# Kernel tuning notes

Measured on AMD Instinct MI355X. Metric: run time of the kernel, lower is better.

Reference implementation:

```python
import jax, jax.numpy as jnp
import numpy as np
import math

HIDDEN = 1024
N_HEADS = 16
N_KV = 4
HEAD_DIM = HIDDEN // N_HEADS  # 64
B, S = 2, 2048
THETA = 100000.0


def _freqs_cos_sin(dim, end, theta):
    # yarn params: original_max_position_embeddings=2048 >= end, so no ramp scaling,
    # attention_factor=1.0 -> plain RoPE frequencies.
    inv = 1.0 / theta ** (np.arange(0, dim, 2)[: dim // 2] / dim)
    t = np.arange(end)
    f = np.outer(t, inv).astype(np.float32)  # (end, dim/2)
    cos = np.concatenate([np.cos(f), np.cos(f)], axis=-1)  # (end, dim)
    sin = np.concatenate([np.sin(f), np.sin(f)], axis=-1)
    return jnp.asarray(cos), jnp.asarray(sin)


def _rotate(x):
    # stack([-x[...,1::2], x[...,::2]], -1).reshape_as(x)
    return jnp.stack([-x[..., 1::2], x[..., ::2]], axis=-1).reshape(x.shape)


def setup_inputs() -> dict:
    key = jax.random.key(0)
    ks = jax.random.split(key, 9)
    s = 0.02
    return {
        "hidden_states": jax.random.normal(ks[0], (B, S, HIDDEN), jnp.float32),
        "attention_mask": jnp.ones((B, S), jnp.int32),
        "Wq": jax.random.normal(ks[1], (HIDDEN, HIDDEN), jnp.float32) * s,
        "bq": jnp.zeros((HIDDEN,), jnp.float32),
        "Wk": jax.random.normal(ks[2], (HIDDEN, N_KV * HEAD_DIM), jnp.float32) * s,
        "bk": jnp.zeros((N_KV * HEAD_DIM,), jnp.float32),
        "Wv": jax.random.normal(ks[3], (HIDDEN, N_KV * HEAD_DIM), jnp.float32) * s,
        "bv": jnp.zeros((N_KV * HEAD_DIM,), jnp.float32),
        "Wo": jax.random.normal(ks[4], (HIDDEN, HIDDEN), jnp.float32) * s,
        "bo": jnp.zeros((HIDDEN,), jnp.float32),
    }


def reference(hidden_states, attention_mask, Wq, bq, Wk, bk, Wv, bv, Wo, bo):
    b, s, _ = hidden_states.shape
    q = (hidden_states @ Wq + bq).reshape(b, s, N_HEADS, HEAD_DIM)
    k = (hidden_states @ Wk + bk).reshape(b, s, N_KV, HEAD_DIM)
    v = (hidden_states @ Wv + bv).reshape(b, s, N_KV, HEAD_DIM)

    cos, sin = _freqs_cos_sin(HEAD_DIM, s, THETA)
    cos = cos[:, None, :]  # (s,1,d) broadcasts over (b,s,h,d)
    sin = sin[:, None, :]
    q = q * cos + _rotate(q) * sin
    k = k * cos + _rotate(k) * sin

    # GQA: repeat_interleave kv heads -> jnp.repeat along head axis
    rep = N_HEADS // N_KV
    k = jnp.repeat(k, rep, axis=2)
    v = jnp.repeat(v, rep, axis=2)

    scores = jnp.einsum("bqhd,bkhd->bhqk", q, k) / math.sqrt(HEAD_DIM)
    neg = jnp.finfo(scores.dtype).min
    causal = jnp.triu(jnp.ones((s, s), bool), k=1)  # (q,kv)
    bias = jnp.where(causal, neg, 0.0).astype(scores.dtype)[None, None]
    key_mask = attention_mask.astype(bool)[:, None, None, :]  # (b,1,1,kv)
    bias = jnp.where(key_mask, bias, neg)
    probs = jax.nn.softmax(scores + bias, axis=-1)
    attn = jnp.einsum("bhqk,bkhd->bqhd", probs, v).reshape(b, s, HIDDEN)
    return attn @ Wo + bo
```

## Files before the change

### kernel.cpp

```cpp
#include <hip/hip_runtime.h>
#include <cstddef>
#include <cstdint>

#define B_   2
#define S_   2048
#define HID  1024
#define NH_  16
#define NKV_ 4
#define DH_  64
#define ROWS (B_ * S_)
#define NQKV 1536
#define QSCALE 0.18033688011112042f

typedef __bf16 bf16_t;
typedef _Float16 f16_t;
typedef bf16_t bf16x8 __attribute__((ext_vector_type(8)));
typedef bf16_t bf16x4 __attribute__((ext_vector_type(4)));
typedef f16_t  f16x8  __attribute__((ext_vector_type(8)));
typedef f16_t  f16x4  __attribute__((ext_vector_type(4)));
typedef float  f32x4  __attribute__((ext_vector_type(4)));

typedef __attribute__((address_space(1))) const uint32_t gu32_t;
typedef __attribute__((address_space(3))) uint32_t lu32_t;

__device__ __forceinline__ void gl_lds16(const void* g, void* l) {
  __builtin_amdgcn_global_load_lds((gu32_t*)g, (lu32_t*)l, 16, 0, 0);
}

__global__ void prep_all(const float* __restrict__ hs,
                         const float* __restrict__ Wq, const float* __restrict__ Wk,
                         const float* __restrict__ Wv, const float* __restrict__ Wo,
                         const float* __restrict__ bq, const float* __restrict__ bk,
                         const float* __restrict__ bv,
                         bf16_t* __restrict__ hsb,
                         bf16_t* __restrict__ Wt, bf16_t* __restrict__ Wot,
                         float* __restrict__ ball, float2* __restrict__ lut)
{
  const int bid = blockIdx.x;
  if (bid < 2048) {
    const int i = (bid * 256 + threadIdx.x) * 8;
    float4 a = *(const float4*)(hs + i);
    float4 b = *(const float4*)(hs + i + 4);
    bf16x8 o;
    o[0]=(bf16_t)a.x; o[1]=(bf16_t)a.y; o[2]=(bf16_t)a.z; o[3]=(bf16_t)a.w;
    o[4]=(bf16_t)b.x; o[5]=(bf16_t)b.y; o[6]=(bf16_t)b.z; o[7]=(bf16_t)b.w;
    *(bf16x8*)(hsb + i) = o;
    return;
  }
  if (bid >= 4614) {
    const int idx = (bid - 4614) * 256 + threadIdx.x;
    const int s = idx >> 5, j = idx & 31;
    const float L = 0.51905126482615037f;
    const float ang = (float)s * exp2f(-L * (float)j);
    lut[idx] = make_float2(cosf(ang), sinf(ang));
    return;
  }
  if (bid >= 4608) {
    int i = (bid - 4608) * 256 + threadIdx.x;
    if (i < NQKV) ball[i] = (i < 1024) ? bq[i] : ((i < 1280) ? bk[i-1024] : bv[i-1280]);
    return;
  }
  const int wb = bid - 2048;
  const float* src; bf16_t* dst; int N, n0, k0;
  if (wb < 1024)      { src = Wq; dst = Wt;            N = 1024; int t = wb;      n0=(t&31)*32; k0=(t>>5)*32; }
  else if (wb < 1280) { src = Wk; dst = Wt + 1024*HID; N = 256;  int t = wb-1024; n0=(t&7)*32;  k0=(t>>3)*32; }
  else if (wb < 1536) { src = Wv; dst = Wt + 1280*HID; N = 256;  int t = wb-1280; n0=(t&7)*32;  k0=(t>>3)*32; }
  else                { src = Wo; dst = Wot;           N = 1024; int t = wb-1536; n0=(t&31)*32; k0=(t>>5)*32; }
  __shared__ bf16_t T[32][33];
  const int tx = threadIdx.x & 31, ty = threadIdx.x >> 5;
#pragma unroll
  for (int i = 0; i < 4; ++i)
    T[ty + i*8][tx] = (bf16_t)src[(size_t)(k0 + ty + i*8) * N + n0 + tx];
  __syncthreads();
#pragma unroll
  for (int i = 0; i < 4; ++i)
    dst[(size_t)(n0 + ty + i*8) * HID + k0 + tx] = T[tx][ty + i*8];
}

__global__ __launch_bounds__(256, 3) void gemm_qkv(
    const bf16_t* __restrict__ A, const bf16_t* __restrict__ Bt,
    const float* __restrict__ bias, const float2* __restrict__ lut,
    bf16_t* __restrict__ C, bf16_t* __restrict__ Kimg, f16_t* __restrict__ Vimg)
{
  __shared__ bf16_t As[2][128 * 64];
  __shared__ bf16_t Bs[2][64 * 64];
  const int tid  = threadIdx.x;
  const int w    = tid >> 6;
  const int lane = tid & 63;
  const int m    = lane & 15;
  const int quad = lane >> 4;
  const int wm   = w >> 1, wn = w & 1;

  const int lin = blockIdx.y * 24 + blockIdx.x;
  const int swz = (lin & 7) * 96 + (lin >> 3);
  const int bx  = swz % 24;
  const int by  = swz / 24;
  const size_t bm = (size_t)by * 128;
  const size_t bn = (size_t)bx * 64;

  const int srow = w * 8 + (lane >> 3);
  const int scol = (lane & 7) * 8;
  const bf16_t* Ag = A  + (bm + srow) * HID + scol;
  const bf16_t* Bg = Bt + (bn + srow) * HID + scol;

  f32x4 acc[4][2];
#pragma unroll
  for (int i = 0; i < 4; ++i)
#pragma unroll
    for (int j = 0; j < 2; ++j) acc[i][j] = (f32x4){0.f, 0.f, 0.f, 0.f};

#pragma unroll
  for (int i = 0; i < 4; ++i)
    gl_lds16(Ag + (size_t)(i * 32) * HID, &As[0][(w * 8 + i * 32) * 64]);
#pragma unroll
  for (int i = 0; i < 2; ++i)
    gl_lds16(Bg + (size_t)(i * 32) * HID, &Bs[0][(w * 8 + i * 32) * 64]);

  int p = 0;
  for (int k0 = 0; k0 < HID; k0 += 64) {
    __syncthreads();
    if (k0 + 64 < HID) {
#pragma unroll
      for (int i = 0; i < 4; ++i)
        gl_lds16(Ag + (size_t)(i * 32) * HID + k0 + 64, &As[p^1][(w * 8 + i * 32) * 64]);
#pragma unroll
      for (int i = 0; i < 2; ++i)
        gl_lds16(Bg + (size_t)(i * 32) * HID + k0 + 64, &Bs[p^1][(w * 8 + i * 32) * 64]);
    }
#pragma unroll
    for (int ks = 0; ks < 2; ++ks) {
      bf16x8 af[4], bfr[2];
#pragma unroll
      for (int mt = 0; mt < 4; ++mt)
        af[mt] = *(const bf16x8*)&As[p][(wm * 64 + mt * 16 + m) * 64 + ks * 32 + quad * 8];
#pragma unroll
      for (int nt = 0; nt < 2; ++nt)
        bfr[nt] = *(const bf16x8*)&Bs[p][(wn * 32 + nt * 16 + m) * 64 + ks * 32 + quad * 8];
#pragma unroll
      for (int mt = 0; mt < 4; ++mt)
#pragma unroll
        for (int nt = 0; nt < 2; ++nt)
          acc[mt][nt] = __builtin_amdgcn_mfma_f32_16x16x32_bf16(bfr[nt], af[mt], acc[mt][nt], 0, 0, 0);
    }
    p ^= 1;
  }

  const int b   = by >> 4;
  const int rt  = by & 15;

  if (bx < 16) {
#pragma unroll
    for (int mt = 0; mt < 4; ++mt) {
      const size_t row = bm + wm * 64 + mt * 16 + m;
#pragma unroll
      for (int nt = 0; nt < 2; ++nt) {
        const size_t col = bn + wn * 32 + nt * 16 + quad * 4;
        float4 bb = *(const float4*)&bias[col];
        bf16x4 o;
        o[0] = (bf16_t)(acc[mt][nt][0] + bb.x);
        o[1] = (bf16_t)(acc[mt][nt][1] + bb.y);
        o[2] = (bf16_t)(acc[mt][nt][2] + bb.z);
        o[3] = (bf16_t)(acc[mt][nt][3] + bb.w);
        *(bf16x4*)&C[row * NQKV + col] = o;
      }
    }
  } else if (bx < 20) {
    const int kvh = bx - 16;
    const size_t img0 = ((size_t)(b * NKV_ + kvh) * 32 + rt * 2) * 4096;
#pragma unroll
    for (int mt = 0; mt < 4; ++mt) {
      const int row128 = wm * 64 + mt * 16 + m;
      const int srw    = rt * 128 + row128;
      const int key    = row128 & 63;
      const size_t img = img0 + (size_t)(row128 >> 6) * 4096;
#pragma unroll
      for (int nt = 0; nt < 2; ++nt) {
        const int d0 = wn * 32 + nt * 16 + quad * 4;
        const float4 bb = *(const float4*)&bias[1024 + kvh * DH_ + d0];
        const float v0 = acc[mt][nt][0] + bb.x;
        const float v1 = acc[mt][nt][1] + bb.y;
        const float v2 = acc[mt][nt][2] + bb.z;
        const float v3 = acc[mt][nt][3] + bb.w;
        const float2* lp = lut + srw * 32 + (d0 & 31);
        const float2 l0 = lp[0], l1 = lp[1], l2 = lp[2], l3 = lp[3];
        bf16x4 o;
        o[0] = (bf16_t)(v0 * l0.x - v1 * l0.y);
        o[1] = (bf16_t)(v1 * l1.x + v0 * l1.y);
        o[2] = (bf16_t)(v2 * l2.x - v3 * l2.y);
        o[3] = (bf16_t)(v3 * l3.x + v2 * l3.y);
        const int slot = (d0 >> 3) ^ (key & 7);
        *(bf16x4*)&Kimg[img + key * 64 + slot * 8 + (d0 & 7)] = o;
      }
    }
  } else {
    const int kvh = bx - 20;
    f16_t* Lv = (f16_t*)&As[0][0];
    __syncthreads();
#pragma unroll
    for (int mt = 0; mt < 4; ++mt) {
      const int row128 = wm * 64 + mt * 16 + m;
#pragma unroll
      for (int nt = 0; nt < 2; ++nt) {
        const int d0 = wn * 32 + nt * 16 + quad * 4;
        const float4 bb = *(const float4*)&bias[1280 + kvh * DH_ + d0];
        f16x4 o;
        o[0] = (f16_t)(acc[mt][nt][0] + bb.x);
        o[1] = (f16_t)(acc[mt][nt][1] + bb.y);
        o[2] = (f16_t)(acc[mt][nt][2] + bb.z);
        o[3] = (f16_t)(acc[mt][nt][3] + bb.w);
        *(f16x4*)&Lv[row128 * 68 + d0] = o;
      }
    }
    __syncthreads();
    const size_t img0 = ((size_t)(b * NKV_ + kvh) * 32 + rt * 2) * 4096;
    const int d  = tid & 63;
    const int qg = tid >> 6;
#pragma unroll
    for (int i = 0; i < 8; ++i) {
      const int ki = i >> 2;
      const int g4 = qg * 4 + (i & 3);
      f16x4 o;
#pragma unroll
      for (int j = 0; j < 4; ++j)
        o[j] = Lv[(ki * 64 + g4 * 4 + j) * 68 + d];
      const int slot = g4 ^ (d & 15);
      *(f16x4*)&Vimg[img0 + (size_t)ki * 4096 + d * 64 + slot * 4] = o;
    }
  }
}

__global__ __launch_bounds__(256, 3) void gemm64_f32o(
    const bf16_t* __restrict__ A, const bf16_t* __restrict__ Bt,
    const float* __restrict__ bias, float* __restrict__ C, int N)
{
  __shared__ bf16_t As[2][128 * 64];
  __shared__ bf16_t Bs[2][64 * 64];
  const int tid  = threadIdx.x;
  const int w    = tid >> 6;
  const int lane = tid & 63;
  const int m    = lane & 15;
  const int quad = lane >> 4;
  const int wm   = w >> 1, wn = w & 1;

  const int lin = blockIdx.y * 16 + blockIdx.x;
  const int swz = (lin & 7) * 64 + (lin >> 3);
  const int bx  = swz & 15;
  const int by  = swz >> 4;
  const size_t bm = (size_t)by * 128;
  const size_t bn = (size_t)bx * 64;

  const int srow = w * 8 + (lane >> 3);
  const int scol = (lane & 7) * 8;
  const bf16_t* Ag = A  + (bm + srow) * HID + scol;
  const bf16_t* Bg = Bt + (bn + srow) * HID + scol;

  f32x4 acc[4][2];
#pragma unroll
  for (int i = 0; i < 4; ++i)
#pragma unroll
    for (int j = 0; j < 2; ++j) acc[i][j] = (f32x4){0.f, 0.f, 0.f, 0.f};

#pragma unroll
  for (int i = 0; i < 4; ++i)
    gl_lds16(Ag + (size_t)(i * 32) * HID, &As[0][(w * 8 + i * 32) * 64]);
#pragma unroll
  for (int i = 0; i < 2; ++i)
    gl_lds16(Bg + (size_t)(i * 32) * HID, &Bs[0][(w * 8 + i * 32) * 64]);

  int p = 0;
  for (int k0 = 0; k0 < HID; k0 += 64) {
    __syncthreads();
    if (k0 + 64 < HID) {
#pragma unroll
      for (int i = 0; i < 4; ++i)
        gl_lds16(Ag + (size_t)(i * 32) * HID + k0 + 64, &As[p^1][(w * 8 + i * 32) * 64]);
#pragma unroll
      for (int i = 0; i < 2; ++i)
        gl_lds16(Bg + (size_t)(i * 32) * HID + k0 + 64, &Bs[p^1][(w * 8 + i * 32) * 64]);
    }
#pragma unroll
    for (int ks = 0; ks < 2; ++ks) {
      bf16x8 af[4], bfr[2];
#pragma unroll
      for (int mt = 0; mt < 4; ++mt)
        af[mt] = *(const bf16x8*)&As[p][(wm * 64 + mt * 16 + m) * 64 + ks * 32 + quad * 8];
#pragma unroll
      for (int nt = 0; nt < 2; ++nt)
        bfr[nt] = *(const bf16x8*)&Bs[p][(wn * 32 + nt * 16 + m) * 64 + ks * 32 + quad * 8];
#pragma unroll
      for (int mt = 0; mt < 4; ++mt)
#pragma unroll
        for (int nt = 0; nt < 2; ++nt)
          acc[mt][nt] = __builtin_amdgcn_mfma_f32_16x16x32_bf16(bfr[nt], af[mt], acc[mt][nt], 0, 0, 0);
    }
    p ^= 1;
  }
#pragma unroll
  for (int mt = 0; mt < 4; ++mt) {
    const size_t row = bm + wm * 64 + mt * 16 + m;
#pragma unroll
    for (int nt = 0; nt < 2; ++nt) {
      const size_t col = bn + wn * 32 + nt * 16 + quad * 4;
      float4 bb = *(const float4*)&bias[col];
      float4 o;
      o.x = acc[mt][nt][0] + bb.x; o.y = acc[mt][nt][1] + bb.y;
      o.z = acc[mt][nt][2] + bb.z; o.w = acc[mt][nt][3] + bb.w;
      *(float4*)&C[row * N + col] = o;
    }
  }
}

#define PROC_TILE(AQ, OACC, LP, Q0W)                                          \
  do {                                                                        \
    f32x4 sc[4];                                                              \
    _Pragma("unroll") for (int cb = 0; cb < 4; ++cb)                          \
      sc[cb] = (f32x4){0.f, 0.f, 0.f, 0.f};                                   \
    _Pragma("unroll") for (int cb = 0; cb < 4; ++cb) {                        \
      const bf16x8 bk0 = *(const bf16x8*)&Ks[g][p][(cb*16 + m) * 64 + x0s * 8]; \
      const bf16x8 bk1 = *(const bf16x8*)&Ks[g][p][(cb*16 + m) * 64 + x1s * 8]; \
      sc[cb] = __builtin_amdgcn_mfma_f32_16x16x32_bf16(bk0, AQ[0], sc[cb], 0, 0, 0); \
      sc[cb] = __builtin_amdgcn_mfma_f32_16x16x32_bf16(bk1, AQ[1], sc[cb], 0, 0, 0); \
    }                                                                         \
    f16x4 bp[4];                                                              \
    {                                                                         \
      const bool needm = (kbase + 63 > (Q0W)) || (mb != ~0ull);               \
      if (needm) {                                                            \
        const int qv = (Q0W) + m;                                             \
        _Pragma("unroll") for (int cb = 0; cb < 4; ++cb)                      \
          _Pragma("unroll") for (int r = 0; r < 4; ++r) {                     \
            const int idx = cb*16 + quad*4 + r;                               \
            const bool ok = (kbase + idx <= qv) && ((mb >> idx) & 1);         \
            sc[cb][r] = ok ? sc[cb][r] : -1e38f;                              \
          }                                                                   \
      }                                                                       \
      float sum = 0.f;                                                        \
      _Pragma("unroll") for (int cb = 0; cb < 4; ++cb) {                      \
        f16x4 pp;                                                             \
        _Pragma("unroll") for (int r = 0; r < 4; ++r) {                       \
          const float pv = __builtin_amdgcn_exp2f(sc[cb][r]);                 \
          sum += pv;                                                          \
          pp[r] = (f16_t)pv;                                                  \
        }                                                                     \
        bp[cb] = pp;                                                          \
      }                                                                       \
      LP += sum;                                                              \
    }                                                                         \
    _Pragma("unroll") for (int cb = 0; cb < 4; ++cb) {                        \
      f16x4 av[4];                                                            \
      _Pragma("unroll") for (int dblk = 0; dblk < 4; ++dblk) {                \
        const int slot = (cb * 4 + quad) ^ m;                                 \
        av[dblk] = *(const f16x4*)&Vs[g][p][(dblk*16 + m) * 64 + slot * 4];   \
      }                                                                       \
      _Pragma("unroll") for (int dblk = 0; dblk < 4; ++dblk)                  \
        OACC[dblk] = __builtin_amdgcn_mfma_f32_16x16x16f16(av[dblk], bp[cb], OACC[dblk], 0, 0, 0); \
    }                                                                         \
  } while (0)

__global__ __launch_bounds__(512, 4) void attn_v11(
    const bf16_t* __restrict__ QKVb, const float2* __restrict__ lut,
    const bf16_t* __restrict__ Kt2, const f16_t* __restrict__ Vt2,
    const int* __restrict__ amask, bf16_t* __restrict__ Ab)
{
  __shared__ __align__(16) bf16_t Ks[2][2][64 * 64];
  __shared__ __align__(16) f16_t  Vs[2][2][64 * 64];

  const int tid  = threadIdx.x;
  const int w    = tid >> 6;
  const int g    = w >> 2;
  const int wl   = w & 3;
  const int lane = tid & 63;
  const int m    = lane & 15;
  const int quad = lane >> 4;
  const int kvh  = blockIdx.y;
  const int b    = blockIdx.z;
  const int h    = kvh * 4 + wl;
  const int x    = blockIdx.x;
  const int q0wA = x * 16;
  const int q0wB = (127 - x) * 16;
  const int nA   = (x >> 2) + 1;
  const int nB   = ((127 - x) >> 2) + 1;
  const int T    = nA + nB;

  bf16x8 aqA[2], aqB[2];
#pragma unroll
  for (int tt = 0; tt < 2; ++tt) {
    const int q0w_t = tt ? q0wB : q0wA;
    const int spos = q0w_t + m;
    const bf16_t* qsrc = QKVb + (size_t)(b * S_ + spos) * NQKV + h * DH_;
    float2 l8[8];
#pragma unroll
    for (int j = 0; j < 8; ++j) l8[j] = lut[spos * 32 + quad * 8 + j];
#pragma unroll
    for (int kc = 0; kc < 2; ++kc) {
      bf16x8 xv = *(const bf16x8*)(qsrc + kc * 32 + quad * 8);
      bf16x8 y;
#pragma unroll
      for (int i = 0; i < 4; ++i) {
        const float x0 = (float)xv[2*i], x1 = (float)xv[2*i+1];
        y[2*i]   = (bf16_t)((x0 * l8[2*i].x   - x1 * l8[2*i].y)   * QSCALE);
        y[2*i+1] = (bf16_t)((x1 * l8[2*i+1].x + x0 * l8[2*i+1].y) * QSCALE);
      }
      if (tt) aqB[kc] = y; else aqA[kc] = y;
    }
  }

  f32x4 oaccA[4], oaccB[4];
#pragma unroll
  for (int d = 0; d < 4; ++d) {
    oaccA[d] = (f32x4){0.f,0.f,0.f,0.f};
    oaccB[d] = (f32x4){0.f,0.f,0.f,0.f};
  }
  float lpA = 0.f, lpB = 0.f;

  const size_t imgbase = ((size_t)(b * NKV_ + kvh) * 32) * 4096;
  const bf16_t* Kg = Kt2 + imgbase;
  const f16_t*  Vg = Vt2 + imgbase;
  const int x0s = quad ^ (m & 7);
  const int x1s = (4 + quad) ^ (m & 7);
  const int* amp = amask + b * S_;

  int mcur;
  {
    const int e0  = g;
    const int kt0 = (e0 >= nA) ? e0 - nA : e0;
    const size_t off = (size_t)kt0 * 4096;
    gl_lds16(Kg + off + (2*wl)   * 512 + lane * 8, &Ks[g][0][(2*wl)   * 512]);
    gl_lds16(Kg + off + (2*wl+1) * 512 + lane * 8, &Ks[g][0][(2*wl+1) * 512]);
    gl_lds16(Vg + off + (2*wl)   * 512 + lane * 8, &Vs[g][0][(2*wl)   * 512]);
    gl_lds16(Vg + off + (2*wl+1) * 512 + lane * 8, &Vs[g][0][(2*wl+1) * 512]);
    mcur = amp[kt0 * 64 + lane];
  }

  int p = 0;
  const int niter = (T + 1) >> 1;
  for (int t = 0; t < niter; ++t) {
    const int e = 2 * t + g;
    __syncthreads();
    const int e2 = e + 2;
    const bool more = (e2 < T);
    int kt2 = 0;
    if (more) {
      kt2 = (e2 >= nA) ? e2 - nA : e2;
      const size_t off = (size_t)kt2 * 4096;
      gl_lds16(Kg + off + (2*wl)   * 512 + lane * 8, &Ks[g][p^1][(2*wl)   * 512]);
      gl_lds16(Kg + off + (2*wl+1) * 512 + lane * 8, &Ks[g][p^1][(2*wl+1) * 512]);
      gl_lds16(Vg + off + (2*wl)   * 512 + lane * 8, &Vs[g][p^1][(2*wl)   * 512]);
      gl_lds16(Vg + off + (2*wl+1) * 512 + lane * 8, &Vs[g][p^1][(2*wl+1) * 512]);
    }
    const int mnext = more ? amp[kt2 * 64 + lane] : 0;
    if (e < T) {
      const uint64_t mb = __ballot(mcur != 0);
      const bool isB = (e >= nA);
      const int kt = isB ? e - nA : e;
      const int kbase = kt * 64;
      if (isB) PROC_TILE(aqB, oaccB, lpB, q0wB);
      else     PROC_TILE(aqA, oaccA, lpA, q0wA);
    }
    mcur = mnext;
    p ^= 1;
  }

  float lAred = lpA;
  lAred += __shfl_xor(lAred, 16); lAred += __shfl_xor(lAred, 32);
  float lBred = lpB;
  lBred += __shfl_xor(lBred, 16); lBred += __shfl_xor(lBred, 32);

  __syncthreads();
  float* scrA = (float*)&Ks[0][0][0];
  float* scrB = (float*)&Vs[0][0][0];
  const int sbase = wl * 1104 + m * 68 + quad * 4;

  if (g == 0) {
#pragma unroll
    for (int dblk = 0; dblk < 4; ++dblk)
      *(f32x4*)&scrA[sbase + dblk * 16] = oaccA[dblk];
    if (quad == 0) scrA[wl * 1104 + 16 * 68 + m] = lAred;
  } else {
#pragma unroll
    for (int dblk = 0; dblk < 4; ++dblk)
      *(f32x4*)&scrB[sbase + dblk * 16] = oaccB[dblk];
    if (quad == 0) scrB[wl * 1104 + 16 * 68 + m] = lBred;
  }
  __syncthreads();

  if (g == 0) {
    const float l = lBred + scrB[wl * 1104 + 16 * 68 + m];
    const float inv = 1.0f / l;
    const size_t row = (size_t)(b * S_ + q0wB + m);
#pragma unroll
    for (int dblk = 0; dblk < 4; ++dblk) {
      const f32x4 part = *(const f32x4*)&scrB[sbase + dblk * 16];
      bf16x4 o;
      o[0] = (bf16_t)((oaccB[dblk][0] + part[0]) * inv);
      o[1] = (bf16_t)((oaccB[dblk][1] + part[1]) * inv);
      o[2] = (bf16_t)((oaccB[dblk][2] + part[2]) * inv);
      o[3] = (bf16_t)((oaccB[dblk][3] + part[3]) * inv);
      *(bf16x4*)&Ab[row * HID + h * DH_ + dblk * 16 + quad * 4] = o;
    }
  } else {
    const float l = lAred + scrA[wl * 1104 + 16 * 68 + m];
    const float inv = 1.0f / l;
    const size_t row = (size_t)(b * S_ + q0wA + m);
#pragma unroll
    for (int dblk = 0; dblk < 4; ++dblk) {
      const f32x4 part = *(const f32x4*)&scrA[sbase + dblk * 16];
      bf16x4 o;
      o[0] = (bf16_t)((oaccA[dblk][0] + part[0]) * inv);
      o[1] = (bf16_t)((oaccA[dblk][1] + part[1]) * inv);
      o[2] = (bf16_t)((oaccA[dblk][2] + part[2]) * inv);
      o[3] = (bf16_t)((oaccA[dblk][3] + part[3]) * inv);
      *(bf16x4*)&Ab[row * HID + h * DH_ + dblk * 16 + quad * 4] = o;
    }
  }
}

extern "C" void kernel_launch(void* const* d_in, const int* in_sizes, int n_in,
                              void* d_out, int out_size, void* d_ws, size_t ws_size,
                              hipStream_t stream)
{
  const float* hs    = (const float*)d_in[0];
  const int*   amask = (const int*)  d_in[1];
  const float* Wq    = (const float*)d_in[2];
  const float* bq    = (const float*)d_in[3];
  const float* Wk    = (const float*)d_in[4];
  const float* bk    = (const float*)d_in[5];
  const float* Wv    = (const float*)d_in[6];
  const float* bv    = (const float*)d_in[7];
  const float* Wo    = (const float*)d_in[8];
  const float* bo    = (const float*)d_in[9];
  float* out = (float*)d_out;

  bf16_t* QKVb = (bf16_t*)d_ws;
  bf16_t* hsb  = QKVb + (size_t)ROWS * NQKV;
  bf16_t* Wt   = hsb + (size_t)ROWS * HID;
  bf16_t* Wot  = Wt + (size_t)NQKV * HID;
  float*  ball = (float*)(Wot + (size_t)HID * HID);
  bf16_t* Kimg = (bf16_t*)(ball + NQKV);
  f16_t*  Vimg = (f16_t*)(Kimg + (size_t)B_*NKV_*32*4096);
  float2* lut  = (float2*)(Vimg + (size_t)B_*NKV_*32*4096);
  bf16_t* Ab   = hsb;

  prep_all<<<4870, 256, 0, stream>>>(hs, Wq, Wk, Wv, Wo, bq, bk, bv,
                                     hsb, Wt, Wot, ball, lut);

  gemm_qkv<<<dim3(NQKV/64, ROWS/128), 256, 0, stream>>>(hsb, Wt, ball, lut,
                                                        QKVb, Kimg, Vimg);

  attn_v11<<<dim3(64, NKV_, B_), 512, 0, stream>>>(QKVb, lut, Kimg, Vimg, amask, Ab);

  gemm64_f32o<<<dim3(HID/64, ROWS/128), 256, 0, stream>>>(Ab, Wot, bo, out, HID);
}
```

Measured before the change: 173.5 us.

## Fuse prep+QKV GEMM and attention+O-proj into persistent kernels with grid barriers

Merges the prep and QKV GEMM kernels into one persistent 768-block kernel that grid-strides over the prep work, waits on an atomic grid barrier, then runs the GEMM. The attention kernel and output projection are likewise fused behind a second grid barrier, with the O-proj retiled to 128x64 tiles using a 2x2 MFMA layout per wave over 512 threads. This removes two kernel launches and their inter-kernel gaps. It relies on every block being co-resident, since a software grid barrier deadlocks otherwise, and it adds spin-wait cost plus a memset launch.

```diff
diff --git a/kernel.cpp b/kernel.cpp
--- a/kernel.cpp
+++ b/kernel.cpp
@@ -27,285 +27,222 @@
   __builtin_amdgcn_global_load_lds((gu32_t*)g, (lu32_t*)l, 16, 0, 0);
 }
 
-__global__ void prep_all(const float* __restrict__ hs,
-                         const float* __restrict__ Wq, const float* __restrict__ Wk,
-                         const float* __restrict__ Wv, const float* __restrict__ Wo,
-                         const float* __restrict__ bq, const float* __restrict__ bk,
-                         const float* __restrict__ bv,
-                         bf16_t* __restrict__ hsb,
-                         bf16_t* __restrict__ Wt, bf16_t* __restrict__ Wot,
-                         float* __restrict__ ball, float2* __restrict__ lut)
+__device__ __forceinline__ void grid_barrier(uint32_t* bar, uint32_t expected) {
+  __syncthreads();
+  if (threadIdx.x == 0) {
+    __threadfence();
+    __hip_atomic_fetch_add(bar, 1u, __ATOMIC_ACQ_REL, __HIP_MEMORY_SCOPE_AGENT);
+    while (__hip_atomic_load(bar, __ATOMIC_ACQUIRE, __HIP_MEMORY_SCOPE_AGENT) < expected)
+      __builtin_amdgcn_s_sleep(8);
+    __threadfence();
+  }
+  __syncthreads();
+}
+
+__global__ __launch_bounds__(256, 3) void fused_prep_qkv(
+    const float* __restrict__ hs,
+    const float* __restrict__ Wq, const float* __restrict__ Wk,
+    const float* __restrict__ Wv, const float* __restrict__ Wo,
+    const float* __restrict__ bq, const float* __restrict__ bk,
+    const float* __restrict__ bv,
+    bf16_t* __restrict__ hsb, bf16_t* __restrict__ Wt, bf16_t* __restrict__ Wot,
+    float* __restrict__ ball, float2* __restrict__ lut,
+    bf16_t* __restrict__ C, bf16_t* __restrict__ Kimg, f16_t* __restrict__ Vimg,
+    uint32_t* __restrict__ bars)
 {
-  const int bid = blockIdx.x;
-  if (bid < 2048) {
-    const int i = (bid * 256 + threadIdx.x) * 8;
-    float4 a = *(const float4*)(hs + i);
-    float4 b = *(const float4*)(hs + i + 4);
-    bf16x8 o;
-    o[0]=(bf16_t)a.x; o[1]=(bf16_t)a.y; o[2]=(bf16_t)a.z; o[3]=(bf16_t)a.w;
-    o[4]=(bf16_t)b.x; o[5]=(bf16_t)b.y; o[6]=(bf16_t)b.z; o[7]=(bf16_t)b.w;
-    *(bf16x8*)(hsb + i) = o;
-    return;
+  __shared__ __align__(16) uint8_t SMEM[49152];
+  const int tid = threadIdx.x;
+
+  {
+    bf16_t (*T)[33] = (bf16_t(*)[33])SMEM;
+    for (int bid = blockIdx.x; bid < 4870; bid += 768) {
+      if (bid < 2048) {
+        const int i = (bid * 256 + tid) * 8;
+        float4 a = *(const float4*)(hs + i);
+        float4 b = *(const float4*)(hs + i + 4);
+        bf16x8 o;
+        o[0]=(bf16_t)a.x; o[1]=(bf16_t)a.y; o[2]=(bf16_t)a.z; o[3]=(bf16_t)a.w;
+        o[4]=(bf16_t)b.x; o[5]=(bf16_t)b.y; o[6]=(bf16_t)b.z; o[7]=(bf16_t)b.w;
+        *(bf16x8*)(hsb + i) = o;
+      } else if (bid >= 4614) {
+        const int idx = (bid - 4614) * 256 + tid;
+        const int s = idx >> 5, j = idx & 31;
+        const float L = 0.51905126482615037f;
+        const float ang = (float)s * exp2f(-L * (float)j);
+        lut[idx] = make_float2(cosf(ang), sinf(ang));
+      } else if (bid >= 4608) {
+        int i = (bid - 4608) * 256 + tid;
+        if (i < NQKV) ball[i] = (i < 1024) ? bq[i] : ((i < 1280) ? bk[i-1024] : bv[i-1280]);
+      } else {
+        const int wb = bid - 2048;
+        const float* src; bf16_t* dst; int N, n0, k0;
+        if (wb < 1024)      { src = Wq; dst = Wt;            N = 1024; int t = wb;      n0=(t&31)*32; k0=(t>>5)*32; }
+        else if (wb < 1280) { src = Wk; dst = Wt + 1024*HID; N = 256;  int t = wb-1024; n0=(t&7)*32;  k0=(t>>3)*32; }
+        else if (wb < 1536) { src = Wv; dst = Wt + 1280*HID; N = 256;  int t = wb-1280; n0=(t&7)*32;  k0=(t>>3)*32; }
+        else                { src = Wo; dst = Wot;           N = 1024; int t = wb-1536; n0=(t&31)*32; k0=(t>>5)*32; }
+        const int tx = tid & 31, ty = tid >> 5;
+#pragma unroll
+        for (int i = 0; i < 4; ++i)
+          T[ty + i*8][tx] = (bf16_t)src[(size_t)(k0 + ty + i*8) * N + n0 + tx];
+        __syncthreads();
+#pragma unroll
+        for (int i = 0; i < 4; ++i)
+          dst[(size_t)(n0 + ty + i*8) * HID + k0 + tx] = T[tx][ty + i*8];
+        __syncthreads();
+      }
+    }
   }
-  if (bid >= 4614) {
-    const int idx = (bid - 4614) * 256 + threadIdx.x;
-    const int s = idx >> 5, j = idx & 31;
-    const float L = 0.51905126482615037f;
-    const float ang = (float)s * exp2f(-L * (float)j);
-    lut[idx] = make_float2(cosf(ang), sinf(ang));
-    return;
-  }
-  if (bid >= 4608) {
-    int i = (bid - 4608) * 256 + threadIdx.x;
-    if (i < NQKV) ball[i] = (i < 1024) ? bq[i] : ((i < 1280) ? bk[i-1024] : bv[i-1280]);
-    return;
-  }
-  const int wb = bid - 2048;
-  const float* src; bf16_t* dst; int N, n0, k0;
-  if (wb < 1024)      { src = Wq; dst = Wt;            N = 1024; int t = wb;      n0=(t&31)*32; k0=(t>>5)*32; }
-  else if (wb < 1280) { src = Wk; dst = Wt + 1024*HID; N = 256;  int t = wb-1024; n0=(t&7)*32;  k0=(t>>3)*32; }
-  else if (wb < 1536) { src = Wv; dst = Wt + 1280*HID; N = 256;  int t = wb-1280; n0=(t&7)*32;  k0=(t>>3)*32; }
-  else                { src = Wo; dst = Wot;           N = 1024; int t = wb-1536; n0=(t&31)*32; k0=(t>>5)*32; }
-  __shared__ bf16_t T[32][33];
-  const int tx = threadIdx.x & 31, ty = threadIdx.x >> 5;
-#pragma unroll
-  for (int i = 0; i < 4; ++i)
-    T[ty + i*8][tx] = (bf16_t)src[(size_t)(k0 + ty + i*8) * N + n0 + tx];
-  __syncthreads();
-#pragma unroll
-  for (int i = 0; i < 4; ++i)
-    dst[(size_t)(n0 + ty + i*8) * HID + k0 + tx] = T[tx][ty + i*8];
-}
-
-__global__ __launch_bounds__(256, 3) void gemm_qkv(
-    const bf16_t* __restrict__ A, const bf16_t* __restrict__ Bt,
-    const float* __restrict__ bias, const float2* __restrict__ lut,
-    bf16_t* __restrict__ C, bf16_t* __restrict__ Kimg, f16_t* __restrict__ Vimg)
-{
-  __shared__ bf16_t As[2][128 * 64];
-  __shared__ bf16_t Bs[2][64 * 64];
-  const int tid  = threadIdx.x;
-  const int w    = tid >> 6;
-  const int lane = tid & 63;
-  const int m    = lane & 15;
-  const int quad = lane >> 4;
-  const int wm   = w >> 1, wn = w & 1;
-
-  const int lin = blockIdx.y * 24 + blockIdx.x;
-  const int swz = (lin & 7) * 96 + (lin >> 3);
-  const int bx  = swz % 24;
-  const int by  = swz / 24;
-  const size_t bm = (size_t)by * 128;
-  const size_t bn = (size_t)bx * 64;
-
-  const int srow = w * 8 + (lane >> 3);
-  const int scol = (lane & 7) * 8;
-  const bf16_t* Ag = A  + (bm + srow) * HID + scol;
-  const bf16_t* Bg = Bt + (bn + srow) * HID + scol;
-
-  f32x4 acc[4][2];
-#pragma unroll
-  for (int i = 0; i < 4; ++i)
-#pragma unroll
-    for (int j = 0; j < 2; ++j) acc[i][j] = (f32x4){0.f, 0.f, 0.f, 0.f};
-
-#pragma unroll
-  for (int i = 0; i < 4; ++i)
-    gl_lds16(Ag + (size_t)(i * 32) * HID, &As[0][(w * 8 + i * 32) * 64]);
-#pragma unroll
-  for (int i = 0; i < 2; ++i)
-    gl_lds16(Bg + (size_t)(i * 32) * HID, &Bs[0][(w * 8 + i * 32) * 64]);
-
-  int p = 0;
-  for (int k0 = 0; k0 < HID; k0 += 64) {
-    __syncthreads();
-    if (k0 + 64 < HID) {
-#pragma unroll
-      for (int i = 0; i < 4; ++i)
-        gl_lds16(Ag + (size_t)(i * 32) * HID + k0 + 64, &As[p^1][(w * 8 + i * 32) * 64]);
-#pragma unroll
-      for (int i = 0; i < 2; ++i)
-        gl_lds16(Bg + (size_t)(i * 32) * HID + k0 + 64, &Bs[p^1][(w * 8 + i * 32) * 64]);
-    }
-#pragma unroll
-    for (int ks = 0; ks < 2; ++ks) {
-      bf16x8 af[4], bfr[2];
-#pragma unroll
-      for (int mt = 0; mt < 4; ++mt)
-        af[mt] = *(const bf16x8*)&As[p][(wm * 64 + mt * 16 + m) * 64 + ks * 32 + quad * 8];
-#pragma unroll
-      for (int nt = 0; nt < 2; ++nt)
-        bfr[nt] = *(const bf16x8*)&Bs[p][(wn * 32 + nt * 16 + m) * 64 + ks * 32 + quad * 8];
-#pragma unroll
-      for (int mt = 0; mt < 4; ++mt)
+
+  grid_barrier(&bars[0], 768u);
+
+  {
+    bf16_t* Asp = (bf16_t*)SMEM;
+    bf16_t* Bsp = (bf16_t*)(SMEM + 32768);
+    const bf16_t* A  = hsb;
+    const bf16_t* Bt = Wt;
+    const float*  bias = ball;
+
+    const int w    = tid >> 6;
+    const int lane = tid & 63;
+    const int m    = lane & 15;
+    const int quad = lane >> 4;
+    const int wm   = w >> 1, wn = w & 1;
+
+    const int lin = blockIdx.x;
+    const int swz = (lin & 7) * 96 + (lin >> 3);
+    const int bx  = swz % 24;
+    const int by  = swz / 24;
+    const size_t bm = (size_t)by * 128;
+    const size_t bn = (size_t)bx * 64;
+
+    const int srow = w * 8 + (lane >> 3);
+    const int scol = (lane & 7) * 8;
+    const bf16_t* Ag = A  + (bm + srow) * HID + scol;
+    const bf16_t* Bg = Bt + (bn + srow) * HID + scol;
+
+    f32x4 acc[4][2];
+#pragma unroll
+    for (int i = 0; i < 4; ++i)
+#pragma unroll
+      for (int j = 0; j < 2; ++j) acc[i][j] = (f32x4){0.f, 0.f, 0.f, 0.f};
+
+#pragma unroll
+    for (int i = 0; i < 4; ++i)
+      gl_lds16(Ag + (size_t)(i * 32) * HID, Asp + (w * 8 + i * 32) * 64);
+#pragma unroll
+    for (int i = 0; i < 2; ++i)
+      gl_lds16(Bg + (size_t)(i * 32) * HID, Bsp + (w * 8 + i * 32) * 64);
+
+    int p = 0;
+    for (int k0 = 0; k0 < HID; k0 += 64) {
+      __syncthreads();
+      if (k0 + 64 < HID) {
+#pragma unroll
+        for (int i = 0; i < 4; ++i)
+          gl_lds16(Ag + (size_t)(i * 32) * HID + k0 + 64, Asp + (p^1) * 8192 + (w * 8 + i * 32) * 64);
+#pragma unroll
+        for (int i = 0; i < 2; ++i)
+          gl_lds16(Bg + (size_t)(i * 32) * HID + k0 + 64, Bsp + (p^1) * 4096 + (w * 8 + i * 32) * 64);
+      }
+#pragma unroll
+      for (int ks = 0; ks < 2; ++ks) {
+        bf16x8 af[4], bfr[2];
+#pragma unroll
+        for (int mt = 0; mt < 4; ++mt)
+          af[mt] = *(const bf16x8*)&Asp[p * 8192 + (wm * 64 + mt * 16 + m) * 64 + ks * 32 + quad * 8];
 #pragma unroll
         for (int nt = 0; nt < 2; ++nt)
-          acc[mt][nt] = __builtin_amdgcn_mfma_f32_16x16x32_bf16(bfr[nt], af[mt], acc[mt][nt], 0, 0, 0);
-    }
-    p ^= 1;
-  }
-
-  const int b   = by >> 4;
-  const int rt  = by & 15;
-
-  if (bx < 16) {
-#pragma unroll
-    for (int mt = 0; mt < 4; ++mt) {
-      const size_t row = bm + wm * 64 + mt * 16 + m;
-#pragma unroll
-      for (int nt = 0; nt < 2; ++nt) {
-        const size_t col = bn + wn * 32 + nt * 16 + quad * 4;
-        float4 bb = *(const float4*)&bias[col];
-        bf16x4 o;
-        o[0] = (bf16_t)(acc[mt][nt][0] + bb.x);
-        o[1] = (bf16_t)(acc[mt][nt][1] + bb.y);
-        o[2] = (bf16_t)(acc[mt][nt][2] + bb.z);
-        o[3] = (bf16_t)(acc[mt][nt][3] + bb.w);
-        *(bf16x4*)&C[row * NQKV + col] = o;
-      }
-    }
-  } else if (bx < 20) {
-    const int kvh = bx - 16;
-    const size_t img0 = ((size_t)(b * NKV_ + kvh) * 32 + rt * 2) * 4096;
-#pragma unroll
-    for (int mt = 0; mt < 4; ++mt) {
-      const int row128 = wm * 64 + mt * 16 + m;
-      const int srw    = rt * 128 + row128;
-      const int key    = row128 & 63;
-      const size_t img = img0 + (size_t)(row128 >> 6) * 4096;
-#pragma unroll
-      for (int nt = 0; nt < 2; ++nt) {
-        const int d0 = wn * 32 + nt * 16 + quad * 4;
-        const float4 bb = *(const float4*)&bias[1024 + kvh * DH_ + d0];
-        const float v0 = acc[mt][nt][0] + bb.x;
-        const float v1 = acc[mt][nt][1] + bb.y;
-        const float v2 = acc[mt][nt][2] + bb.z;
-        const float v3 = acc[mt][nt][3] + bb.w;
-        const float2* lp = lut + srw * 32 + (d0 & 31);
-        const float2 l0 = lp[0], l1 = lp[1], l2 = lp[2], l3 = lp[3];
-        bf16x4 o;
-        o[0] = (bf16_t)(v0 * l0.x - v1 * l0.y);
-        o[1] = (bf16_t)(v1 * l1.x + v0 * l1.y);
-        o[2] = (bf16_t)(v2 * l2.x - v3 * l2.y);
-        o[3] = (bf16_t)(v3 * l3.x + v2 * l3.y);
-        const int slot = (d0 >> 3) ^ (key & 7);
-        *(bf16x4*)&Kimg[img + key * 64 + slot * 8 + (d0 & 7)] = o;
-      }
-    }
-  } else {
-    const int kvh = bx - 20;
-    f16_t* Lv = (f16_t*)&As[0][0];
-    __syncthreads();
-#pragma unroll
-    for (int mt = 0; mt < 4; ++mt) {
-      const int row128 = wm * 64 + mt * 16 + m;
-#pragma unroll
-      for (int nt = 0; nt < 2; ++nt) {
-        const int d0 = wn * 32 + nt * 16 + quad * 4;
-        const float4 bb = *(const float4*)&bias[1280 + kvh * DH_ + d0];
+          bfr[nt] = *(const bf16x8*)&Bsp[p * 4096 + (wn * 32 + nt * 16 + m) * 64 + ks * 32 + quad * 8];
+#pragma unroll
+        for (int mt = 0; mt < 4; ++mt)
+#pragma unroll
+          for (int nt = 0; nt < 2; ++nt)
+            acc[mt][nt] = __builtin_amdgcn_mfma_f32_16x16x32_bf16(bfr[nt], af[mt], acc[mt][nt], 0, 0, 0);
+      }
+      p ^= 1;
+    }
+
+    const int b   = by >> 4;
+    const int rt  = by & 15;
+
+    if (bx < 16) {
+#pragma unroll
+      for (int mt = 0; mt < 4; ++mt) {
+        const size_t row = bm + wm * 64 + mt * 16 + m;
+#pragma unroll
+        for (int nt = 0; nt < 2; ++nt) {
+          const size_t col = bn + wn * 32 + nt * 16 + quad * 4;
+          float4 bb = *(const float4*)&bias[col];
+          bf16x4 o;
+          o[0] = (bf16_t)(acc[mt][nt][0] + bb.x);
+          o[1] = (bf16_t)(acc[mt][nt][1] + bb.y);
+          o[2] = (bf16_t)(acc[mt][nt][2] + bb.z);
+          o[3] = (bf16_t)(acc[mt][nt][3] + bb.w);
+          *(bf16x4*)&C[row * NQKV + col] = o;
+        }
+      }
+    } else if (bx < 20) {
+      const int kvh = bx - 16;
+      const size_t img0 = ((size_t)(b * NKV_ + kvh) * 32 + rt * 2) * 4096;
+#pragma unroll
+      for (int mt = 0; mt < 4; ++mt) {
+        const int row128 = wm * 64 + mt * 16 + m;
+        const int srw    = rt * 128 + row128;
+        const int key    = row128 & 63;
+        const size_t img = img0 + (size_t)(row128 >> 6) * 4096;
+#pragma unroll
+        for (int nt = 0; nt < 2; ++nt) {
+          const int d0 = wn * 32 + nt * 16 + quad * 4;
+          const float4 bb = *(const float4*)&bias[1024 + kvh * DH_ + d0];
+          const float v0 = acc[mt][nt][0] + bb.x;
+          const float v1 = acc[mt][nt][1] + bb.y;
+          const float v2 = acc[mt][nt][2] + bb.z;
+          const float v3 = acc[mt][nt][3] + bb.w;
+          const float2* lp = lut + srw * 32 + (d0 & 31);
+          const float2 l0 = lp[0], l1 = lp[1], l2 = lp[2], l3 = lp[3];
+          bf16x4 o;
+          o[0] = (bf16_t)(v0 * l0.x - v1 * l0.y);
+          o[1] = (bf16_t)(v1 * l1.x + v0 * l1.y);
+          o[2] = (bf16_t)(v2 * l2.x - v3 * l2.y);
+          o[3] = (bf16_t)(v3 * l3.x + v2 * l3.y);
+          const int slot = (d0 >> 3) ^ (key & 7);
+          *(bf16x4*)&Kimg[img + key * 64 + slot * 8 + (d0 & 7)] = o;
+        }
+      }
+    } else {
+      const int kvh = bx - 20;
+      f16_t* Lv = (f16_t*)SMEM;
+      __syncthreads();
+#pragma unroll
+      for (int mt = 0; mt < 4; ++mt) {
+        const int row128 = wm * 64 + mt * 16 + m;
+#pragma unroll
+        for (int nt = 0; nt < 2; ++nt) {
+          const int d0 = wn * 32 + nt * 16 + quad * 4;
+          const float4 bb = *(const float4*)&bias[1280 + kvh * DH_ + d0];
+          f16x4 o;
+          o[0] = (f16_t)(acc[mt][nt][0] + bb.x);
+          o[1] = (f16_t)(acc[mt][nt][1] + bb.y);
+          o[2] = (f16_t)(acc[mt][nt][2] + bb.z);
+          o[3] = (f16_t)(acc[mt][nt][3] + bb.w);
+          *(f16x4*)&Lv[row128 * 68 + d0] = o;
+        }
+      }
+      __syncthreads();
+      const size_t img0 = ((size_t)(b * NKV_ + kvh) * 32 + rt * 2) * 4096;
+      const int d  = tid & 63;
+      const int qg = tid >> 6;
+#pragma unroll
+      for (int i = 0; i < 8; ++i) {
+        const int ki = i >> 2;
+        const int g4 = qg * 4 + (i & 3);
         f16x4 o;
-        o[0] = (f16_t)(acc[mt][nt][0] + bb.x);
-        o[1] = (f16_t)(acc[mt][nt][1] + bb.y);
-        o[2] = (f16_t)(acc[mt][nt][2] + bb.z);
-        o[3] = (f16_t)(acc[mt][nt][3] + bb.w);
-        *(f16x4*)&Lv[row128 * 68 + d0] = o;
-      }
-    }
-    __syncthreads();
-    const size_t img0 = ((size_t)(b * NKV_ + kvh) * 32 + rt * 2) * 4096;
-    const int d  = tid & 63;
-    const int qg = tid >> 6;
-#pragma unroll
-    for (int i = 0; i < 8; ++i) {
-      const int ki = i >> 2;
-      const int g4 = qg * 4 + (i & 3);
-      f16x4 o;
-#pragma unroll
-      for (int j = 0; j < 4; ++j)
-        o[j] = Lv[(ki * 64 + g4 * 4 + j) * 68 + d];
-      const int slot = g4 ^ (d & 15);
-      *(f16x4*)&Vimg[img0 + (size_t)ki * 4096 + d * 64 + slot * 4] = o;
-    }
-  }
-}
-
-__global__ __launch_bounds__(256, 3) void gemm64_f32o(
-    const bf16_t* __restrict__ A, const bf16_t* __restrict__ Bt,
-    const float* __restrict__ bias, float* __restrict__ C, int N)
-{
-  __shared__ bf16_t As[2][128 * 64];
-  __shared__ bf16_t Bs[2][64 * 64];
-  const int tid  = threadIdx.x;
-  const int w    = tid >> 6;
-  const int lane = tid & 63;
-  const int m    = lane & 15;
-  const int quad = lane >> 4;
-  const int wm   = w >> 1, wn = w & 1;
-
-  const int lin = blockIdx.y * 16 + blockIdx.x;
-  const int swz = (lin & 7) * 64 + (lin >> 3);
-  const int bx  = swz & 15;
-  const int by  = swz >> 4;
-  const size_t bm = (size_t)by * 128;
-  const size_t bn = (size_t)bx * 64;
-
-  const int srow = w * 8 + (lane >> 3);
-  const int scol = (lane & 7) * 8;
-  const bf16_t* Ag = A  + (bm + srow) * HID + scol;
-  const bf16_t* Bg = Bt + (bn + srow) * HID + scol;
-
-  f32x4 acc[4][2];
-#pragma unroll
-  for (int i = 0; i < 4; ++i)
-#pragma unroll
-    for (int j = 0; j < 2; ++j) acc[i][j] = (f32x4){0.f, 0.f, 0.f, 0.f};
-
-#pragma unroll
-  for (int i = 0; i < 4; ++i)
-    gl_lds16(Ag + (size_t)(i * 32) * HID, &As[0][(w * 8 + i * 32) * 64]);
-#pragma unroll
-  for (int i = 0; i < 2; ++i)
-    gl_lds16(Bg + (size_t)(i * 32) * HID, &Bs[0][(w * 8 + i * 32) * 64]);
-
-  int p = 0;
-  for (int k0 = 0; k0 < HID; k0 += 64) {
-    __syncthreads();
-    if (k0 + 64 < HID) {
-#pragma unroll
-      for (int i = 0; i < 4; ++i)
-        gl_lds16(Ag + (size_t)(i * 32) * HID + k0 + 64, &As[p^1][(w * 8 + i * 32) * 64]);
-#pragma unroll
-      for (int i = 0; i < 2; ++i)
-        gl_lds16(Bg + (size_t)(i * 32) * HID + k0 + 64, &Bs[p^1][(w * 8 + i * 32) * 64]);
-    }
-#pragma unroll
-    for (int ks = 0; ks < 2; ++ks) {
-      bf16x8 af[4], bfr[2];
-#pragma unroll
-      for (int mt = 0; mt < 4; ++mt)
-        af[mt] = *(const bf16x8*)&As[p][(wm * 64 + mt * 16 + m) * 64 + ks * 32 + quad * 8];
-#pragma unroll
-      for (int nt = 0; nt < 2; ++nt)
-        bfr[nt] = *(const bf16x8*)&Bs[p][(wn * 32 + nt * 16 + m) * 64 + ks * 32 + quad * 8];
-#pragma unroll
-      for (int mt = 0; mt < 4; ++mt)
-#pragma unroll
-        for (int nt = 0; nt < 2; ++nt)
-          acc[mt][nt] = __builtin_amdgcn_mfma_f32_16x16x32_bf16(bfr[nt], af[mt], acc[mt][nt], 0, 0, 0);
-    }
-    p ^= 1;
-  }
-#pragma unroll
-  for (int mt = 0; mt < 4; ++mt) {
-    const size_t row = bm + wm * 64 + mt * 16 + m;
-#pragma unroll
-    for (int nt = 0; nt < 2; ++nt) {
-      const size_t col = bn + wn * 32 + nt * 16 + quad * 4;
-      float4 bb = *(const float4*)&bias[col];
-      float4 o;
-      o.x = acc[mt][nt][0] + bb.x; o.y = acc[mt][nt][1] + bb.y;
-      o.z = acc[mt][nt][2] + bb.z; o.w = acc[mt][nt][3] + bb.w;
-      *(float4*)&C[row * N + col] = o;
+#pragma unroll
+        for (int j = 0; j < 4; ++j)
+          o[j] = Lv[(ki * 64 + g4 * 4 + j) * 68 + d];
+        const int slot = g4 ^ (d & 15);
+        *(f16x4*)&Vimg[img0 + (size_t)ki * 4096 + d * 64 + slot * 4] = o;
+      }
     }
   }
 }
@@ -316,8 +253,8 @@
     _Pragma("unroll") for (int cb = 0; cb < 4; ++cb)                          \
       sc[cb] = (f32x4){0.f, 0.f, 0.f, 0.f};                                   \
     _Pragma("unroll") for (int cb = 0; cb < 4; ++cb) {                        \
-      const bf16x8 bk0 = *(const bf16x8*)&Ks[g][p][(cb*16 + m) * 64 + x0s * 8]; \
-      const bf16x8 bk1 = *(const bf16x8*)&Ks[g][p][(cb*16 + m) * 64 + x1s * 8]; \
+      const bf16x8 bk0 = *(const bf16x8*)&Ksp[(g*2+p)*4096 + (cb*16 + m) * 64 + x0s * 8]; \
+      const bf16x8 bk1 = *(const bf16x8*)&Ksp[(g*2+p)*4096 + (cb*16 + m) * 64 + x1s * 8]; \
       sc[cb] = __builtin_amdgcn_mfma_f32_16x16x32_bf16(bk0, AQ[0], sc[cb], 0, 0, 0); \
       sc[cb] = __builtin_amdgcn_mfma_f32_16x16x32_bf16(bk1, AQ[1], sc[cb], 0, 0, 0); \
     }                                                                         \
@@ -349,167 +286,242 @@
       f16x4 av[4];                                                            \
       _Pragma("unroll") for (int dblk = 0; dblk < 4; ++dblk) {                \
         const int slot = (cb * 4 + quad) ^ m;                                 \
-        av[dblk] = *(const f16x4*)&Vs[g][p][(dblk*16 + m) * 64 + slot * 4];   \
+        av[dblk] = *(const f16x4*)&Vsp[(g*2+p)*4096 + (dblk*16 + m) * 64 + slot * 4]; \
       }                                                                       \
       _Pragma("unroll") for (int dblk = 0; dblk < 4; ++dblk)                  \
         OACC[dblk] = __builtin_amdgcn_mfma_f32_16x16x16f16(av[dblk], bp[cb], OACC[dblk], 0, 0, 0); \
     }                                                                         \
   } while (0)
 
-__global__ __launch_bounds__(512, 4) void attn_v11(
+__global__ __launch_bounds__(512, 4) void fused_attn_o(
     const bf16_t* __restrict__ QKVb, const float2* __restrict__ lut,
     const bf16_t* __restrict__ Kt2, const f16_t* __restrict__ Vt2,
-    const int* __restrict__ amask, bf16_t* __restrict__ Ab)
+    const int* __restrict__ amask, bf16_t* __restrict__ Ab,
+    const bf16_t* __restrict__ Wot, const float* __restrict__ bo,
+    float* __restrict__ out, uint32_t* __restrict__ bars)
 {
-  __shared__ __align__(16) bf16_t Ks[2][2][64 * 64];
-  __shared__ __align__(16) f16_t  Vs[2][2][64 * 64];
+  __shared__ __align__(16) uint8_t SMEM[65536];
+  bf16_t* Ksp = (bf16_t*)SMEM;
+  f16_t*  Vsp = (f16_t*)(SMEM + 32768);
 
   const int tid  = threadIdx.x;
   const int w    = tid >> 6;
-  const int g    = w >> 2;
-  const int wl   = w & 3;
   const int lane = tid & 63;
   const int m    = lane & 15;
   const int quad = lane >> 4;
   const int kvh  = blockIdx.y;
   const int b    = blockIdx.z;
-  const int h    = kvh * 4 + wl;
   const int x    = blockIdx.x;
-  const int q0wA = x * 16;
-  const int q0wB = (127 - x) * 16;
-  const int nA   = (x >> 2) + 1;
-  const int nB   = ((127 - x) >> 2) + 1;
-  const int T    = nA + nB;
-
-  bf16x8 aqA[2], aqB[2];
-#pragma unroll
-  for (int tt = 0; tt < 2; ++tt) {
-    const int q0w_t = tt ? q0wB : q0wA;
-    const int spos = q0w_t + m;
-    const bf16_t* qsrc = QKVb + (size_t)(b * S_ + spos) * NQKV + h * DH_;
-    float2 l8[8];
-#pragma unroll
-    for (int j = 0; j < 8; ++j) l8[j] = lut[spos * 32 + quad * 8 + j];
-#pragma unroll
-    for (int kc = 0; kc < 2; ++kc) {
-      bf16x8 xv = *(const bf16x8*)(qsrc + kc * 32 + quad * 8);
-      bf16x8 y;
-#pragma unroll
-      for (int i = 0; i < 4; ++i) {
-        const float x0 = (float)xv[2*i], x1 = (float)xv[2*i+1];
-        y[2*i]   = (bf16_t)((x0 * l8[2*i].x   - x1 * l8[2*i].y)   * QSCALE);
-        y[2*i+1] = (bf16_t)((x1 * l8[2*i+1].x + x0 * l8[2*i+1].y) * QSCALE);
-      }
-      if (tt) aqB[kc] = y; else aqA[kc] = y;
+
+  {
+    const int g    = w >> 2;
+    const int wl   = w & 3;
+    const int h    = kvh * 4 + wl;
+    const int q0wA = x * 16;
+    const int q0wB = (127 - x) * 16;
+    const int nA   = (x >> 2) + 1;
+    const int nB   = ((127 - x) >> 2) + 1;
+    const int T    = nA + nB;
+
+    bf16x8 aqA[2], aqB[2];
+#pragma unroll
+    for (int tt = 0; tt < 2; ++tt) {
+      const int q0w_t = tt ? q0wB : q0wA;
+      const int spos = q0w_t + m;
+      const bf16_t* qsrc = QKVb + (size_t)(b * S_ + spos) * NQKV + h * DH_;
+      float2 l8[8];
+#pragma unroll
+      for (int j = 0; j < 8; ++j) l8[j] = lut[spos * 32 + quad * 8 + j];
+#pragma unroll
+      for (int kc = 0; kc < 2; ++kc) {
+        bf16x8 xv = *(const bf16x8*)(qsrc + kc * 32 + quad * 8);
+        bf16x8 y;
+#pragma unroll
+        for (int i = 0; i < 4; ++i) {
+          const float x0 = (float)xv[2*i], x1 = (float)xv[2*i+1];
+          y[2*i]   = (bf16_t)((x0 * l8[2*i].x   - x1 * l8[2*i].y)   * QSCALE);
+          y[2*i+1] = (bf16_t)((x1 * l8[2*i+1].x + x0 * l8[2*i+1].y) * QSCALE);
+        }
+        if (tt) aqB[kc] = y; else aqA[kc] = y;
+      }
+    }
+
+    f32x4 oaccA[4], oaccB[4];
+#pragma unroll
+    for (int d = 0; d < 4; ++d) {
+      oaccA[d] = (f32x4){0.f,0.f,0.f,0.f};
+      oaccB[d] = (f32x4){0.f,0.f,0.f,0.f};
+    }
+    float lpA = 0.f, lpB = 0.f;
+
+    const size_t imgbase = ((size_t)(b * NKV_ + kvh) * 32) * 4096;
+    const bf16_t* Kg = Kt2 + imgbase;
+    const f16_t*  Vg = Vt2 + imgbase;
+    const int x0s = quad ^ (m & 7);
+    const int x1s = (4 + quad) ^ (m & 7);
+    const int* amp = amask + b * S_;
+
+    int mcur;
+    {
+      const int e0  = g;
+      const int kt0 = (e0 >= nA) ? e0 - nA : e0;
+      const size_t off = (size_t)kt0 * 4096;
+      gl_lds16(Kg + off + (2*wl)   * 512 + lane * 8, Ksp + (g*2)*4096 + (2*wl)   * 512);
+      gl_lds16(Kg + off + (2*wl+1) * 512 + lane * 8, Ksp + (g*2)*4096 + (2*wl+1) * 512);
+      gl_lds16(Vg + off + (2*wl)   * 512 + lane * 8, Vsp + (g*2)*4096 + (2*wl)   * 512);
+      gl_lds16(Vg + off + (2*wl+1) * 512 + lane * 8, Vsp + (g*2)*4096 + (2*wl+1) * 512);
+      mcur = amp[kt0 * 64 + lane];
+    }
+
+    int p = 0;
+    for (int t = 0; t < 17; ++t) {
+      const int e = 2 * t + g;
+      __syncthreads();
+      const int e2 = e + 2;
+      const bool more = (e2 < T);
+      int kt2 = 0;
+      if (more) {
+        kt2 = (e2 >= nA) ? e2 - nA : e2;
+        const size_t off = (size_t)kt2 * 4096;
+        gl_lds16(Kg + off + (2*wl)   * 512 + lane * 8, Ksp + (g*2 + (p^1))*4096 + (2*wl)   * 512);
+        gl_lds16(Kg + off + (2*wl+1) * 512 + lane * 8, Ksp + (g*2 + (p^1))*4096 + (2*wl+1) * 512);
+        gl_lds16(Vg + off + (2*wl)   * 512 + lane * 8, Vsp + (g*2 + (p^1))*4096 + (2*wl)   * 512);
+        gl_lds16(Vg + off + (2*wl+1) * 512 + lane * 8, Vsp + (g*2 + (p^1))*4096 + (2*wl+1) * 512);
+      }
+      const int mnext = more ? amp[kt2 * 64 + lane] : 0;
+      if (e < T) {
+        const uint64_t mb = __ballot(mcur != 0);
+        const bool isB = (e >= nA);
+        const int kt = isB ? e - nA : e;
+        const int kbase = kt * 64;
+        if (isB) PROC_TILE(aqB, oaccB, lpB, q0wB);
+        else     PROC_TILE(aqA, oaccA, lpA, q0wA);
+      }
+      mcur = mnext;
+      p ^= 1;
+    }
+
+    float lAred = lpA;
+    lAred += __shfl_xor(lAred, 16); lAred += __shfl_xor(lAred, 32);
+    float lBred = lpB;
+    lBred += __shfl_xor(lBred, 16); lBred += __shfl_xor(lBred, 32);
+
+    __syncthreads();
+    float* scrA = (float*)SMEM;
+    float* scrB = (float*)(SMEM + 32768);
+    const int sbase = wl * 1104 + m * 68 + quad * 4;
+
+    if (g == 0) {
+#pragma unroll
+      for (int dblk = 0; dblk < 4; ++dblk)
+        *(f32x4*)&scrA[sbase + dblk * 16] = oaccA[dblk];
+      if (quad == 0) scrA[wl * 1104 + 16 * 68 + m] = lAred;
+    } else {
+#pragma unroll
+      for (int dblk = 0; dblk < 4; ++dblk)
+        *(f32x4*)&scrB[sbase + dblk * 16] = oaccB[dblk];
+      if (quad == 0) scrB[wl * 1104 + 16 * 68 + m] = lBred;
+    }
+    __syncthreads();
+
+    if (g == 0) {
+      const float l = lBred + scrB[wl * 1104 + 16 * 68 + m];
+      const float inv = 1.0f / l;
+      const size_t row = (size_t)(b * S_ + q0wB + m);
+#pragma unroll
+      for (int dblk = 0; dblk < 4; ++dblk) {
+        const f32x4 part = *(const f32x4*)&scrB[sbase + dblk * 16];
+        bf16x4 o;
+        o[0] = (bf16_t)((oaccB[dblk][0] + part[0]) * inv);
+        o[1] = (bf16_t)((oaccB[dblk][1] + part[1]) * inv);
+        o[2] = (bf16_t)((oaccB[dblk][2] + part[2]) * inv);
+        o[3] = (bf16_t)((oaccB[dblk][3] + part[3]) * inv);
+        *(bf16x4*)&Ab[row * HID + h * DH_ + dblk * 16 + quad * 4] = o;
+      }
+    } else {
+      const float l = lAred + scrA[wl * 1104 + 16 * 68 + m];
+      const float inv = 1.0f / l;
+      const size_t row = (size_t)(b * S_ + q0wA + m);
+#pragma unroll
+      for (int dblk = 0; dblk < 4; ++dblk) {
+        const f32x4 part = *(const f32x4*)&scrA[sbase + dblk * 16];
+        bf16x4 o;
+        o[0] = (bf16_t)((oaccA[dblk][0] + part[0]) * inv);
+        o[1] = (bf16_t)((oaccA[dblk][1] + part[1]) * inv);
+        o[2] = (bf16_t)((oaccA[dblk][2] + part[2]) * inv);
+        o[3] = (bf16_t)((oaccA[dblk][3] + part[3]) * inv);
+        *(bf16x4*)&Ab[row * HID + h * DH_ + dblk * 16 + quad * 4] = o;
+      }
     }
   }
 
-  f32x4 oaccA[4], oaccB[4];
-#pragma unroll
-  for (int d = 0; d < 4; ++d) {
-    oaccA[d] = (f32x4){0.f,0.f,0.f,0.f};
-    oaccB[d] = (f32x4){0.f,0.f,0.f,0.f};
-  }
-  float lpA = 0.f, lpB = 0.f;
-
-  const size_t imgbase = ((size_t)(b * NKV_ + kvh) * 32) * 4096;
-  const bf16_t* Kg = Kt2 + imgbase;
-  const f16_t*  Vg = Vt2 + imgbase;
-  const int x0s = quad ^ (m & 7);
-  const int x1s = (4 + quad) ^ (m & 7);
-  const int* amp = amask + b * S_;
-
-  int mcur;
+  grid_barrier(&bars[1], 512u);
+
   {
-    const int e0  = g;
-    const int kt0 = (e0 >= nA) ? e0 - nA : e0;
-    const size_t off = (size_t)kt0 * 4096;
-    gl_lds16(Kg + off + (2*wl)   * 512 + lane * 8, &Ks[g][0][(2*wl)   * 512]);
-    gl_lds16(Kg + off + (2*wl+1) * 512 + lane * 8, &Ks[g][0][(2*wl+1) * 512]);
-    gl_lds16(Vg + off + (2*wl)   * 512 + lane * 8, &Vs[g][0][(2*wl)   * 512]);
-    gl_lds16(Vg + off + (2*wl+1) * 512 + lane * 8, &Vs[g][0][(2*wl+1) * 512]);
-    mcur = amp[kt0 * 64 + lane];
-  }
-
-  int p = 0;
-  const int niter = (T + 1) >> 1;
-  for (int t = 0; t < niter; ++t) {
-    const int e = 2 * t + g;
-    __syncthreads();
-    const int e2 = e + 2;
-    const bool more = (e2 < T);
-    int kt2 = 0;
-    if (more) {
-      kt2 = (e2 >= nA) ? e2 - nA : e2;
-      const size_t off = (size_t)kt2 * 4096;
-      gl_lds16(Kg + off + (2*wl)   * 512 + lane * 8, &Ks[g][p^1][(2*wl)   * 512]);
-      gl_lds16(Kg + off + (2*wl+1) * 512 + lane * 8, &Ks[g][p^1][(2*wl+1) * 512]);
-      gl_lds16(Vg + off + (2*wl)   * 512 + lane * 8, &Vs[g][p^1][(2*wl)   * 512]);
-      gl_lds16(Vg + off + (2*wl+1) * 512 + lane * 8, &Vs[g][p^1][(2*wl+1) * 512]);
-    }
-    const int mnext = more ? amp[kt2 * 64 + lane] : 0;
-    if (e < T) {
-      const uint64_t mb = __ballot(mcur != 0);
-      const bool isB = (e >= nA);
-      const int kt = isB ? e - nA : e;
-      const int kbase = kt * 64;
-      if (isB) PROC_TILE(aqB, oaccB, lpB, q0wB);
-      else     PROC_TILE(aqA, oaccA, lpA, q0wA);
-    }
-    mcur = mnext;
-    p ^= 1;
-  }
-
-  float lAred = lpA;
-  lAred += __shfl_xor(lAred, 16); lAred += __shfl_xor(lAred, 32);
-  float lBred = lpB;
-  lBred += __shfl_xor(lBred, 16); lBred += __shfl_xor(lBred, 32);
-
-  __syncthreads();
-  float* scrA = (float*)&Ks[0][0][0];
-  float* scrB = (float*)&Vs[0][0][0];
-  const int sbase = wl * 1104 + m * 68 + quad * 4;
-
-  if (g == 0) {
-#pragma unroll
-    for (int dblk = 0; dblk < 4; ++dblk)
-      *(f32x4*)&scrA[sbase + dblk * 16] = oaccA[dblk];
-    if (quad == 0) scrA[wl * 1104 + 16 * 68 + m] = lAred;
-  } else {
-#pragma unroll
-    for (int dblk = 0; dblk < 4; ++dblk)
-      *(f32x4*)&scrB[sbase + dblk * 16] = oaccB[dblk];
-    if (quad == 0) scrB[wl * 1104 + 16 * 68 + m] = lBred;
-  }
-  __syncthreads();
-
-  if (g == 0) {
-    const float l = lBred + scrB[wl * 1104 + 16 * 68 + m];
-    const float inv = 1.0f / l;
-    const size_t row = (size_t)(b * S_ + q0wB + m);
-#pragma unroll
-    for (int dblk = 0; dblk < 4; ++dblk) {
-      const f32x4 part = *(const f32x4*)&scrB[sbase + dblk * 16];
-      bf16x4 o;
-      o[0] = (bf16_t)((oaccB[dblk][0] + part[0]) * inv);
-      o[1] = (bf16_t)((oaccB[dblk][1] + part[1]) * inv);
-      o[2] = (bf16_t)((oaccB[dblk][2] + part[2]) * inv);
-      o[3] = (bf16_t)((oaccB[dblk][3] + part[3]) * inv);
-      *(bf16x4*)&Ab[row * HID + h * DH_ + dblk * 16 + quad * 4] = o;
-    }
-  } else {
-    const float l = lAred + scrA[wl * 1104 + 16 * 68 + m];
-    const float inv = 1.0f / l;
-    const size_t row = (size_t)(b * S_ + q0wA + m);
-#pragma unroll
-    for (int dblk = 0; dblk < 4; ++dblk) {
-      const f32x4 part = *(const f32x4*)&scrA[sbase + dblk * 16];
-      bf16x4 o;
-      o[0] = (bf16_t)((oaccA[dblk][0] + part[0]) * inv);
-      o[1] = (bf16_t)((oaccA[dblk][1] + part[1]) * inv);
-      o[2] = (bf16_t)((oaccA[dblk][2] + part[2]) * inv);
-      o[3] = (bf16_t)((oaccA[dblk][3] + part[3]) * inv);
-      *(bf16x4*)&Ab[row * HID + h * DH_ + dblk * 16 + quad * 4] = o;
+    bf16_t* Asp = (bf16_t*)SMEM;
+    bf16_t* Bsp = (bf16_t*)(SMEM + 32768);
+
+    const int lin = (b * 4 + kvh) * 64 + x;
+    const int swz = (lin & 7) * 64 + (lin >> 3);
+    const int bx2 = swz & 15;
+    const int by2 = swz >> 4;
+    const size_t bm = (size_t)by2 * 128;
+    const size_t bn = (size_t)bx2 * 64;
+
+    const int wm = w >> 1;
+    const int wn = w & 1;
+    const int sr   = lane >> 3;
+    const int scol = (lane & 7) * 8;
+    const bf16_t* Ag = Ab  + (bm + w * 16 + sr) * HID + scol;
+    const bf16_t* Bg = Wot + (bn + w * 8  + sr) * HID + scol;
+
+    f32x4 acc[2][2];
+#pragma unroll
+    for (int i = 0; i < 2; ++i)
+#pragma unroll
+      for (int j = 0; j < 2; ++j) acc[i][j] = (f32x4){0.f, 0.f, 0.f, 0.f};
+
+    gl_lds16(Ag,           Asp + (w * 16)     * 64);
+    gl_lds16(Ag + 8 * HID, Asp + (w * 16 + 8) * 64);
+    gl_lds16(Bg,           Bsp + (w * 8)      * 64);
+
+    int p = 0;
+    for (int k0 = 0; k0 < HID; k0 += 64) {
+      __syncthreads();
+      if (k0 + 64 < HID) {
+        gl_lds16(Ag + k0 + 64,           Asp + (p^1) * 8192 + (w * 16)     * 64);
+        gl_lds16(Ag + 8 * HID + k0 + 64, Asp + (p^1) * 8192 + (w * 16 + 8) * 64);
+        gl_lds16(Bg + k0 + 64,           Bsp + (p^1) * 4096 + (w * 8)      * 64);
+      }
+#pragma unroll
+      for (int ks = 0; ks < 2; ++ks) {
+        bf16x8 af[2], bfr[2];
+#pragma unroll
+        for (int mt = 0; mt < 2; ++mt)
+          af[mt] = *(const bf16x8*)&Asp[p * 8192 + (wm * 32 + mt * 16 + m) * 64 + ks * 32 + quad * 8];
+#pragma unroll
+        for (int nt = 0; nt < 2; ++nt)
+          bfr[nt] = *(const bf16x8*)&Bsp[p * 4096 + (wn * 32 + nt * 16 + m) * 64 + ks * 32 + quad * 8];
+#pragma unroll
+        for (int mt = 0; mt < 2; ++mt)
+#pragma unroll
+          for (int nt = 0; nt < 2; ++nt)
+            acc[mt][nt] = __builtin_amdgcn_mfma_f32_16x16x32_bf16(bfr[nt], af[mt], acc[mt][nt], 0, 0, 0);
+      }
+      p ^= 1;
+    }
+#pragma unroll
+    for (int mt = 0; mt < 2; ++mt) {
+      const size_t row = bm + wm * 32 + mt * 16 + m;
+#pragma unroll
+      for (int nt = 0; nt < 2; ++nt) {
+        const size_t col = bn + wn * 32 + nt * 16 + quad * 4;
+        float4 bb = *(const float4*)&bo[col];
+        float4 o;
+        o.x = acc[mt][nt][0] + bb.x; o.y = acc[mt][nt][1] + bb.y;
+        o.z = acc[mt][nt][2] + bb.z; o.w = acc[mt][nt][3] + bb.w;
+        *(float4*)&out[row * HID + col] = o;
+      }
     }
   }
 }
@@ -538,15 +550,15 @@
   bf16_t* Kimg = (bf16_t*)(ball + NQKV);
   f16_t*  Vimg = (f16_t*)(Kimg + (size_t)B_*NKV_*32*4096);
   float2* lut  = (float2*)(Vimg + (size_t)B_*NKV_*32*4096);
+  uint32_t* bars = (uint32_t*)(lut + 65536);
   bf16_t* Ab   = hsb;
 
-  prep_all<<<4870, 256, 0, stream>>>(hs, Wq, Wk, Wv, Wo, bq, bk, bv,
-                                     hsb, Wt, Wot, ball, lut);
-
-  gemm_qkv<<<dim3(NQKV/64, ROWS/128), 256, 0, stream>>>(hsb, Wt, ball, lut,
-                                                        QKVb, Kimg, Vimg);
-
-  attn_v11<<<dim3(64, NKV_, B_), 512, 0, stream>>>(QKVb, lut, Kimg, Vimg, amask, Ab);
-
-  gemm64_f32o<<<dim3(HID/64, ROWS/128), 256, 0, stream>>>(Ab, Wot, bo, out, HID);
+  hipMemsetAsync(bars, 0, 2 * sizeof(uint32_t), stream);
+
+  fused_prep_qkv<<<768, 256, 0, stream>>>(hs, Wq, Wk, Wv, Wo, bq, bk, bv,
+                                          hsb, Wt, Wot, ball, lut,
+                                          QKVb, Kimg, Vimg, bars);
+
+  fused_attn_o<<<dim3(64, NKV_, B_), 512, 0, stream>>>(QKVb, lut, Kimg, Vimg,
+                                                       amask, Ab, Wot, bo, out, bars);
 }
```

New measurement: 360.4 us. 2.08x slower.
